# Performance work log

Measured on AMD Instinct MI355X. Metric: run time of the kernel, lower is better.

## Reference

```python
import jax, jax.numpy as jnp
import numpy as np

T, D_IN, H, KV, HD = 1024, 2048, 32, 8, 64
GROUP = H // KV  # 4
EPS = 1e-6


def _rmsnorm(x, w):
    inv_rms = jax.lax.rsqrt(jnp.mean(x * x, axis=-1, keepdims=True) + EPS)
    return x * inv_rms * w


def _rope(x, cos, sin):
    # x: [heads, T, HD]; cos/sin: [T, HD]
    hd = x.shape[-1]
    x1, x2 = x[..., : hd // 2], x[..., hd // 2 :]
    rotated = jnp.concatenate([-x2, x1], axis=-1)
    return x * cos[None, :, :] + rotated * sin[None, :, :]


def setup_inputs() -> dict:
    key = jax.random.key(0)
    ks = jax.random.split(key, 6)
    x = jax.random.normal(ks[0], (T, D_IN), dtype=jnp.float32)
    # RoPE tables (cos/sin over [T, HD])
    inv_freq = 1.0 / (10000.0 ** (np.arange(0, HD, 2, dtype=np.float64) / HD))
    ang = np.arange(T, dtype=np.float64)[:, None] * inv_freq[None, :]
    emb = np.concatenate([ang, ang], axis=-1)
    cos = jnp.asarray(np.cos(emb), dtype=jnp.float32)
    sin = jnp.asarray(np.sin(emb), dtype=jnp.float32)
    # causal mask: True above diagonal -> masked to -inf
    mask = jnp.triu(jnp.ones((T, T), dtype=jnp.bool_), k=1)
    # kaiming_normal fan_in (relu): std = sqrt(2/fan_in)
    Wq = jax.random.normal(ks[1], (H * HD, D_IN), jnp.float32) * (2.0 / D_IN) ** 0.5
    Wk = jax.random.normal(ks[2], (KV * HD, D_IN), jnp.float32) * (2.0 / D_IN) ** 0.5
    Wv = jax.random.normal(ks[3], (KV * HD, D_IN), jnp.float32) * (2.0 / D_IN) ** 0.5
    Wo = jax.random.normal(ks[4], (D_IN, H * HD), jnp.float32) * (2.0 / (H * HD)) ** 0.5
    q_norm_w = jnp.ones((HD,), jnp.float32)
    k_norm_w = jnp.ones((HD,), jnp.float32)
    one = jnp.ones((1,), jnp.float32)
    return {
        "x": x, "scale_x": one, "mask": mask,
        "cos": cos, "scale_cos": one, "sin": sin, "scale_sin": one,
        "Wq": Wq, "Wk": Wk, "Wv": Wv, "Wo": Wo,
        "q_norm_w": q_norm_w, "k_norm_w": k_norm_w,
    }


def reference(x, scale_x, mask, cos, scale_cos, sin, scale_sin,
              Wq, Wk, Wv, Wo, q_norm_w, k_norm_w):
    num_tokens = x.shape[0]
    # QKV projections
    q = (x @ Wq.T).reshape(num_tokens, H, HD).transpose(1, 0, 2)   # [H, T, HD]
    k = (x @ Wk.T).reshape(num_tokens, KV, HD).transpose(1, 0, 2)  # [KV, T, HD]
    v = (x @ Wv.T).reshape(num_tokens, KV, HD).transpose(1, 0, 2)  # [KV, T, HD]
    # qk_norm
    q = _rmsnorm(q, q_norm_w)
    k = _rmsnorm(k, k_norm_w)
    # RoPE
    q = _rope(q, cos, sin)
    k = _rope(k, cos, sin)
    # expand KV groups to all heads (repeat_interleave along head axis)
    k = jnp.repeat(k, GROUP, axis=0)  # [H, T, HD]
    v = jnp.repeat(v, GROUP, axis=0)  # [H, T, HD]
    # attention scores
    qk = jnp.einsum("htd,hsd->hts", q, k) / (HD ** 0.5)
    qk = jnp.where(mask[None, :, :], -jnp.inf, qk)
    attn = jax.nn.softmax(qk, axis=-1)
    out = jnp.einsum("hts,hsd->htd", attn, v)          # [H, T, HD]
    out = out.transpose(1, 0, 2).reshape(num_tokens, H * HD)
    return out @ Wo.T  # [T, D_IN]
```

## Files before the change

### kernel.cpp

```cpp
#include <hip/hip_runtime.h>

typedef __bf16 bf16x8 __attribute__((ext_vector_type(8)));
typedef float f32x4 __attribute__((ext_vector_type(4)));

#define T_TOK 1024
#define DIN   2048
#define NH    32
#define NKV   8
#define HD    64

__device__ __forceinline__ unsigned short f2bf(float f) {
  unsigned int u = __float_as_uint(f);
  unsigned int r = (u + 0x7fffu + ((u >> 16) & 1u)) >> 16;
  return (unsigned short)r;
}

__device__ __forceinline__ void glds16(const void* g, void* lds) {
  __builtin_amdgcn_global_load_lds(
      (const __attribute__((address_space(1))) void*)g,
      (__attribute__((address_space(3))) void*)lds, 16, 0, 0);
}

__global__ __launch_bounds__(256) void k_cvt_all(
    const float* __restrict__ x,  const float* __restrict__ wq,
    const float* __restrict__ wk, const float* __restrict__ wv,
    const float* __restrict__ wo, unsigned short* __restrict__ xb,
    unsigned short* __restrict__ wqkv, unsigned short* __restrict__ wob) {
  const long NX = 1l << 21, NWQ = 1l << 22, NWK = 1l << 20, NWV = 1l << 20;
  long i4 = ((long)blockIdx.x * blockDim.x + threadIdx.x) * 4;
  const float* src;
  unsigned short* dst;
  long off;
  if (i4 < NX)                       { src = x;  dst = xb;   off = i4; }
  else if (i4 < NX + NWQ)            { src = wq; dst = wqkv; off = i4 - NX; }
  else if (i4 < NX + NWQ + NWK)      { src = wk; dst = wqkv + NWQ; off = i4 - NX - NWQ; }
  else if (i4 < NX + NWQ + NWK + NWV){ src = wv; dst = wqkv + NWQ + NWK; off = i4 - NX - NWQ - NWK; }
  else                               { src = wo; dst = wob;  off = i4 - NX - NWQ - NWK - NWV; }
  float4 v = *reinterpret_cast<const float4*>(src + off);
  ushort4 o;
  o.x = f2bf(v.x); o.y = f2bf(v.y); o.z = f2bf(v.z); o.w = f2bf(v.w);
  *reinterpret_cast<ushort4*>(dst + off) = o;
}

template<int BM, int BN>
__global__ __launch_bounds__(256) void k_gemm2(
    const unsigned short* __restrict__ A, const unsigned short* __restrict__ B,
    float* __restrict__ C, int N, int K) {
  constexpr int NI = BM / 32;
  constexpr int NJ = BN / 32;
  __shared__ unsigned short As[2][BM * 64];
  __shared__ unsigned short Bs[2][BN * 64];
  const int lane = threadIdx.x & 63;
  const int wave = threadIdx.x >> 6;
  const int wm = wave >> 1, wn = wave & 1;
  const int lr = lane & 15, lk = lane >> 4;
  const int brow = blockIdx.y * BM;
  const int bcol = blockIdx.x * BN;

  const int srow = lane >> 3;
  const int scol = ((lane & 7) ^ srow) * 8;
  const unsigned short* Ag = A + (long)(brow + srow) * K + scol;
  const unsigned short* Bg = B + (long)(bcol + srow) * K + scol;

  f32x4 acc[NI][NJ];
#pragma unroll
  for (int i = 0; i < NI; i++)
#pragma unroll
    for (int j = 0; j < NJ; j++) acc[i][j] = (f32x4){0.f, 0.f, 0.f, 0.f};

  const int swz = (lr & 7) << 4;
  const int nt = K / 64;
  int cur = 0;

#pragma unroll
  for (int i = 0; i < NI; i++) {
    int strip = i * 4 + wave;
    glds16(Ag + (long)strip * 8 * K, (char*)As[0] + strip * 1024);
  }
#pragma unroll
  for (int i = 0; i < NJ; i++) {
    int strip = i * 4 + wave;
    glds16(Bg + (long)strip * 8 * K, (char*)Bs[0] + strip * 1024);
  }
  __syncthreads();

  for (int t = 0; t < nt; t++) {
    if (t + 1 < nt) {
      const int kk = (t + 1) * 64;
#pragma unroll
      for (int i = 0; i < NI; i++) {
        int strip = i * 4 + wave;
        glds16(Ag + (long)strip * 8 * K + kk, (char*)As[cur ^ 1] + strip * 1024);
      }
#pragma unroll
      for (int i = 0; i < NJ; i++) {
        int strip = i * 4 + wave;
        glds16(Bg + (long)strip * 8 * K + kk, (char*)Bs[cur ^ 1] + strip * 1024);
      }
    }
#pragma unroll
    for (int s = 0; s < 2; s++) {
      bf16x8 a[NI], b[NJ];
#pragma unroll
      for (int i = 0; i < NI; i++) {
        int row = wm * (BM / 2) + i * 16 + lr;
        a[i] = *reinterpret_cast<const bf16x8*>(
            (const char*)As[cur] + row * 128 + ((s * 64 + lk * 16) ^ swz));
      }
#pragma unroll
      for (int j = 0; j < NJ; j++) {
        int row = wn * (BN / 2) + j * 16 + lr;
        b[j] = *reinterpret_cast<const bf16x8*>(
            (const char*)Bs[cur] + row * 128 + ((s * 64 + lk * 16) ^ swz));
      }
#pragma unroll
      for (int i = 0; i < NI; i++)
#pragma unroll
        for (int j = 0; j < NJ; j++)
          acc[i][j] = __builtin_amdgcn_mfma_f32_16x16x32_bf16(a[i], b[j], acc[i][j], 0, 0, 0);
    }
    __syncthreads();
    cur ^= 1;
  }

#pragma unroll
  for (int i = 0; i < NI; i++)
#pragma unroll
    for (int j = 0; j < NJ; j++)
#pragma unroll
      for (int p = 0; p < 4; p++)
        C[(long)(brow + wm * (BM / 2) + i * 16 + lk * 4 + p) * N +
          (bcol + wn * (BN / 2) + j * 16 + lr)] = acc[i][j][p];
}

__global__ void k_norm_rope(const float* __restrict__ qkv_lin,
                            unsigned short* __restrict__ qb, unsigned short* __restrict__ kb,
                            const float* __restrict__ cosT, const float* __restrict__ sinT,
                            const float* __restrict__ qw, const float* __restrict__ kw) {
  int gw = (blockIdx.x * blockDim.x + threadIdx.x) >> 6;
  int lane = threadIdx.x & 63;
  int t = gw / (NH + NKV);
  int hh = gw % (NH + NKV);
  if (t >= T_TOK) return;
  const float* base;
  unsigned short* ob;
  const float* w;
  if (hh < NH) {
    base = qkv_lin + (long)t * 3072 + hh * HD;
    ob   = qb + (long)t * (NH * HD) + hh * HD;
    w = qw;
  } else {
    int kh = hh - NH;
    base = qkv_lin + (long)t * 3072 + 2048 + kh * HD;
    ob   = kb + (long)t * (NKV * HD) + kh * HD;
    w = kw;
  }
  float v = base[lane];
  float ss = v * v;
#pragma unroll
  for (int off = 1; off < 64; off <<= 1) ss += __shfl_xor(ss, off);
  float xn = v * rsqrtf(ss * (1.0f / HD) + 1e-6f) * w[lane];
  float other = __shfl_xor(xn, 32);
  float c = cosT[t * HD + lane], s = sinT[t * HD + lane];
  ob[lane] = f2bf(xn * c + (lane < 32 ? -other : other) * s);
}

__global__ __launch_bounds__(256) void k_vt(const float* __restrict__ qkv_lin,
                                            unsigned short* __restrict__ out) {
  __shared__ float t[32][33];
  int tx = threadIdx.x & 31, ty = threadIdx.x >> 5;
  int r0 = blockIdx.y * 32;
  int c0 = blockIdx.x * 32;
#pragma unroll
  for (int r = 0; r < 4; r++)
    t[ty + r * 8][tx] = qkv_lin[(long)(r0 + ty + r * 8) * 3072 + 2560 + c0 + tx];
  __syncthreads();
#pragma unroll
  for (int r = 0; r < 4; r++)
    out[(long)(c0 + ty + r * 8) * 1024 + r0 + tx] = f2bf(t[tx][ty + r * 8]);
}

__global__ __launch_bounds__(256) void k_flash(
    const unsigned short* __restrict__ qb, const unsigned short* __restrict__ kb,
    const unsigned short* __restrict__ vtb, unsigned short* __restrict__ ao) {
  __shared__ unsigned short Ks[2][64 * 64];
  __shared__ unsigned short Vs[2][64 * 64];
  __shared__ unsigned short plds[4][16 * 64];
  const int rb = 63 - blockIdx.x;
  const int kvh = blockIdx.y;
  const int lane = threadIdx.x & 63;
  const int wave = threadIdx.x >> 6;
  const int h = kvh * 4 + wave;
  const int lr = lane & 15, lk = lane >> 4;
  const int qrow = rb * 16;
  const int qt = rb >> 2;
  const int qrel = (rb & 3) * 16 + lr;
  const int pswz = (lr & 7) << 4;
  char* pbase = (char*)plds[wave];
  const float SC = 0.125f * 1.44269504f;
  const f32x4 z4 = {0.f, 0.f, 0.f, 0.f};

  const int srow = lane >> 3;
  const int scol = ((lane & 7) ^ srow) * 8;

#define STAGE(buf, tt) do {                                                    \
    _Pragma("unroll") for (int s_ = 0; s_ < 2; s_++) {                         \
      int strip = s_ * 4 + wave;                                               \
      glds16(kb + (long)((tt) * 64 + strip * 8 + srow) * 512 + kvh * 64 + scol,\
             (char*)Ks[buf] + strip * 1024);                                   \
      glds16(vtb + (long)(kvh * 64 + strip * 8 + srow) * 1024 + (tt) * 64 + scol,\
             (char*)Vs[buf] + strip * 1024);                                   \
    }                                                                          \
  } while (0)

  const unsigned short* qp = qb + (long)(qrow + lr) * (NH * HD) + h * HD + lk * 8;
  bf16x8 qa0 = *reinterpret_cast<const bf16x8*>(qp);
  bf16x8 qa1 = *reinterpret_cast<const bf16x8*>(qp + 32);

  f32x4 o[4];
#pragma unroll
  for (int f = 0; f < 4; f++) o[f] = z4;
  float m2 = -3.0e38f;
  float lp = 0.f;

  const int ntiles = qt + 1;
  int cur = 0;
  STAGE(0, 0);
  __syncthreads();

  for (int t = 0; t < ntiles; t++) {
    if (t + 1 < ntiles) STAGE(cur ^ 1, t + 1);
    bf16x8 kf0[4], kf1[4];
#pragma unroll
    for (int f = 0; f < 4; f++) {
      const char* kbase = (const char*)Ks[cur] + (f * 16 + lr) * 128;
      kf0[f] = *reinterpret_cast<const bf16x8*>(kbase + ((lk * 16) ^ pswz));
      kf1[f] = *reinterpret_cast<const bf16x8*>(kbase + ((64 + lk * 16) ^ pswz));
    }
    f32x4 sacc[4];
    __builtin_amdgcn_s_setprio(1);
#pragma unroll
    for (int f = 0; f < 4; f++) {
      sacc[f] = __builtin_amdgcn_mfma_f32_16x16x32_bf16(kf0[f], qa0, z4, 0, 0, 0);
      sacc[f] = __builtin_amdgcn_mfma_f32_16x16x32_bf16(kf1[f], qa1, sacc[f], 0, 0, 0);
    }
    __builtin_amdgcn_s_setprio(0);
    const bool diag = (t == qt);
    float tmax = -3.0e38f;
#pragma unroll
    for (int f = 0; f < 4; f++)
#pragma unroll
      for (int p = 0; p < 4; p++) {
        float s_ = sacc[f][p] * SC;
        if (diag && (f * 16 + lk * 4 + p) > qrel) s_ = -3.0e38f;
        sacc[f][p] = s_;
        tmax = fmaxf(tmax, s_);
      }
    tmax = fmaxf(tmax, __shfl_xor(tmax, 16));
    tmax = fmaxf(tmax, __shfl_xor(tmax, 32));
    float mn = fmaxf(m2, tmax);
    float r = exp2f(m2 - mn);
    m2 = mn;
    float rp[4];
#pragma unroll
    for (int p = 0; p < 4; p++)
      rp[p] = __shfl(r, (lane & 48) | (lk * 4 + p));
    float ps = 0.f;
#pragma unroll
    for (int f = 0; f < 4; f++) {
      float e0 = exp2f(sacc[f][0] - mn), e1 = exp2f(sacc[f][1] - mn);
      float e2 = exp2f(sacc[f][2] - mn), e3 = exp2f(sacc[f][3] - mn);
      ps += (e0 + e1) + (e2 + e3);
      uint2 pk;
      pk.x = (unsigned)f2bf(e0) | ((unsigned)f2bf(e1) << 16);
      pk.y = (unsigned)f2bf(e2) | ((unsigned)f2bf(e3) << 16);
      *reinterpret_cast<uint2*>(pbase + lr * 128 + ((f * 32 + lk * 8) ^ pswz)) = pk;
    }
    lp = lp * r + ps;
#pragma unroll
    for (int fd = 0; fd < 4; fd++)
#pragma unroll
      for (int p = 0; p < 4; p++) o[fd][p] *= rp[p];
    bf16x8 vfr[8];
#pragma unroll
    for (int fd = 0; fd < 4; fd++) {
      const char* vbase = (const char*)Vs[cur] + (fd * 16 + lr) * 128;
      vfr[fd]     = *reinterpret_cast<const bf16x8*>(vbase + ((lk * 16) ^ pswz));
      vfr[4 + fd] = *reinterpret_cast<const bf16x8*>(vbase + ((64 + lk * 16) ^ pswz));
    }
    __builtin_amdgcn_s_setprio(1);
#pragma unroll
    for (int ks = 0; ks < 2; ks++) {
      bf16x8 pa = *reinterpret_cast<const bf16x8*>(
          pbase + lr * 128 + ((ks * 64 + lk * 16) ^ pswz));
#pragma unroll
      for (int fd = 0; fd < 4; fd++)
        o[fd] = __builtin_amdgcn_mfma_f32_16x16x32_bf16(pa, vfr[ks * 4 + fd], o[fd], 0, 0, 0);
    }
    __builtin_amdgcn_s_setprio(0);
    __syncthreads();
    cur ^= 1;
  }

  lp += __shfl_xor(lp, 16);
  lp += __shfl_xor(lp, 32);
  float lo[4];
#pragma unroll
  for (int p = 0; p < 4; p++) lo[p] = __shfl(lp, (lane & 48) | (lk * 4 + p));
#pragma unroll
  for (int fd = 0; fd < 4; fd++)
#pragma unroll
    for (int p = 0; p < 4; p++) {
      int qg = qrow + lk * 4 + p;
      int d = fd * 16 + lr;
      ao[(long)qg * (NH * HD) + h * HD + d] = f2bf(o[fd][p] / lo[p]);
    }
#undef STAGE
}

extern "C" void kernel_launch(void* const* d_in, const int* in_sizes, int n_in,
                              void* d_out, int out_size, void* d_ws, size_t ws_size,
                              hipStream_t stream) {
  const float* x    = (const float*)d_in[0];
  const float* cosT = (const float*)d_in[3];
  const float* sinT = (const float*)d_in[5];
  const float* Wq   = (const float*)d_in[7];
  const float* Wk   = (const float*)d_in[8];
  const float* Wv   = (const float*)d_in[9];
  const float* Wo   = (const float*)d_in[10];
  const float* qw   = (const float*)d_in[11];
  const float* kw   = (const float*)d_in[12];
  float* out = (float*)d_out;

  char* ws = (char*)d_ws;
  unsigned short* xb    = (unsigned short*)(ws);
  unsigned short* Wqkv  = (unsigned short*)(ws + (4u << 20));
  unsigned short* Wob   = (unsigned short*)(ws + (16u << 20));
  float* qkv_lin = (float*)(ws + (24u << 20));
  unsigned short* qbb = (unsigned short*)(ws + (36u << 20));
  unsigned short* kbb = (unsigned short*)(ws + (40u << 20));
  unsigned short* vtb = (unsigned short*)(ws + (41u << 20));
  unsigned short* ao  = (unsigned short*)(ws + (42u << 20));

  k_cvt_all<<<12288, 256, 0, stream>>>(x, Wq, Wk, Wv, Wo, xb, Wqkv, Wob);

  k_gemm2<128, 128><<<dim3(24, 8), 256, 0, stream>>>(xb, Wqkv, qkv_lin, 3072, 2048);

  k_norm_rope<<<(T_TOK * (NH + NKV) * 64) / 256, 256, 0, stream>>>(
      qkv_lin, qbb, kbb, cosT, sinT, qw, kw);

  k_vt<<<dim3(16, 32), 256, 0, stream>>>(qkv_lin, vtb);

  k_flash<<<dim3(64, 8), 256, 0, stream>>>(qbb, kbb, vtb, ao);

  k_gemm2<128, 128><<<dim3(16, 8), 256, 0, stream>>>(ao, Wob, out, 2048, 2048);
}
```

Before: 220.7 us.

## Deepen GEMM and flash-attention LDS pipelines to four buffers with explicit vmcnt waits

Both the bf16 GEMM and the flash-attention kernel move from double-buffered to 4-slot LDS ring buffers with three tiles prefetched ahead. The per-iteration __syncthreads is replaced by explicit s_waitcnt vmcnt counts plus a single s_barrier, so later async loads can stay in flight while the current tile is computed. MFMA sections get raised wave priority. This hides more global-load latency at the cost of doubled LDS usage, and it relies on the hand-set vmcnt values matching the exact number of issued loads.

```diff
diff --git a/kernel.cpp b/kernel.cpp
--- a/kernel.cpp
+++ b/kernel.cpp
@@ -43,13 +43,13 @@
 }
 
 template<int BM, int BN>
-__global__ __launch_bounds__(256) void k_gemm2(
+__global__ __launch_bounds__(256) void k_gemm3(
     const unsigned short* __restrict__ A, const unsigned short* __restrict__ B,
     float* __restrict__ C, int N, int K) {
   constexpr int NI = BM / 32;
   constexpr int NJ = BN / 32;
-  __shared__ unsigned short As[2][BM * 64];
-  __shared__ unsigned short Bs[2][BN * 64];
+  __shared__ unsigned short As[4][BM * 64];
+  __shared__ unsigned short Bs[4][BN * 64];
   const int lane = threadIdx.x & 63;
   const int wave = threadIdx.x >> 6;
   const int wm = wave >> 1, wn = wave & 1;
@@ -70,34 +70,31 @@
 
   const int swz = (lr & 7) << 4;
   const int nt = K / 64;
-  int cur = 0;
-
-#pragma unroll
-  for (int i = 0; i < NI; i++) {
-    int strip = i * 4 + wave;
-    glds16(Ag + (long)strip * 8 * K, (char*)As[0] + strip * 1024);
-  }
-#pragma unroll
-  for (int i = 0; i < NJ; i++) {
-    int strip = i * 4 + wave;
-    glds16(Bg + (long)strip * 8 * K, (char*)Bs[0] + strip * 1024);
-  }
-  __syncthreads();
+
+#define GSTAGE(buf, tt) do {                                                   \
+    const int kk_ = (tt) * 64;                                                 \
+    _Pragma("unroll") for (int i_ = 0; i_ < NI; i_++) {                        \
+      int strip = i_ * 4 + wave;                                               \
+      glds16(Ag + (long)strip * 8 * K + kk_, (char*)As[buf] + strip * 1024);   \
+    }                                                                          \
+    _Pragma("unroll") for (int i_ = 0; i_ < NJ; i_++) {                        \
+      int strip = i_ * 4 + wave;                                               \
+      glds16(Bg + (long)strip * 8 * K + kk_, (char*)Bs[buf] + strip * 1024);   \
+    }                                                                          \
+  } while (0)
+
+  GSTAGE(0, 0);
+  GSTAGE(1, 1);
+  GSTAGE(2, 2);
 
   for (int t = 0; t < nt; t++) {
-    if (t + 1 < nt) {
-      const int kk = (t + 1) * 64;
-#pragma unroll
-      for (int i = 0; i < NI; i++) {
-        int strip = i * 4 + wave;
-        glds16(Ag + (long)strip * 8 * K + kk, (char*)As[cur ^ 1] + strip * 1024);
-      }
-#pragma unroll
-      for (int i = 0; i < NJ; i++) {
-        int strip = i * 4 + wave;
-        glds16(Bg + (long)strip * 8 * K + kk, (char*)Bs[cur ^ 1] + strip * 1024);
-      }
-    }
+    if (t + 2 < nt)      { asm volatile("s_waitcnt vmcnt(16)" ::: "memory"); }
+    else if (t + 1 < nt) { asm volatile("s_waitcnt vmcnt(8)"  ::: "memory"); }
+    else                 { asm volatile("s_waitcnt vmcnt(0)"  ::: "memory"); }
+    __builtin_amdgcn_sched_barrier(0);
+    __builtin_amdgcn_s_barrier();
+    if (t + 3 < nt) GSTAGE((t + 3) & 3, t + 3);
+    const int cur = t & 3;
 #pragma unroll
     for (int s = 0; s < 2; s++) {
       bf16x8 a[NI], b[NJ];
@@ -113,15 +110,16 @@
         b[j] = *reinterpret_cast<const bf16x8*>(
             (const char*)Bs[cur] + row * 128 + ((s * 64 + lk * 16) ^ swz));
       }
+      __builtin_amdgcn_s_setprio(1);
 #pragma unroll
       for (int i = 0; i < NI; i++)
 #pragma unroll
         for (int j = 0; j < NJ; j++)
           acc[i][j] = __builtin_amdgcn_mfma_f32_16x16x32_bf16(a[i], b[j], acc[i][j], 0, 0, 0);
-    }
-    __syncthreads();
-    cur ^= 1;
+      __builtin_amdgcn_s_setprio(0);
+    }
   }
+#undef GSTAGE
 
 #pragma unroll
   for (int i = 0; i < NI; i++)
@@ -183,8 +181,8 @@
 __global__ __launch_bounds__(256) void k_flash(
     const unsigned short* __restrict__ qb, const unsigned short* __restrict__ kb,
     const unsigned short* __restrict__ vtb, unsigned short* __restrict__ ao) {
-  __shared__ unsigned short Ks[2][64 * 64];
-  __shared__ unsigned short Vs[2][64 * 64];
+  __shared__ unsigned short Ks[4][64 * 64];
+  __shared__ unsigned short Vs[4][64 * 64];
   __shared__ unsigned short plds[4][16 * 64];
   const int rb = 63 - blockIdx.x;
   const int kvh = blockIdx.y;
@@ -224,12 +222,18 @@
   float lp = 0.f;
 
   const int ntiles = qt + 1;
-  int cur = 0;
   STAGE(0, 0);
-  __syncthreads();
+  if (ntiles > 1) STAGE(1, 1);
+  if (ntiles > 2) STAGE(2, 2);
 
   for (int t = 0; t < ntiles; t++) {
-    if (t + 1 < ntiles) STAGE(cur ^ 1, t + 1);
+    if (t + 2 < ntiles)      { asm volatile("s_waitcnt vmcnt(8)" ::: "memory"); }
+    else if (t + 1 < ntiles) { asm volatile("s_waitcnt vmcnt(4)" ::: "memory"); }
+    else                     { asm volatile("s_waitcnt vmcnt(0)" ::: "memory"); }
+    __builtin_amdgcn_sched_barrier(0);
+    __builtin_amdgcn_s_barrier();
+    if (t + 3 < ntiles) STAGE((t + 3) & 3, t + 3);
+    const int cur = t & 3;
     bf16x8 kf0[4], kf1[4];
 #pragma unroll
     for (int f = 0; f < 4; f++) {
@@ -298,9 +302,8 @@
         o[fd] = __builtin_amdgcn_mfma_f32_16x16x32_bf16(pa, vfr[ks * 4 + fd], o[fd], 0, 0, 0);
     }
     __builtin_amdgcn_s_setprio(0);
-    __syncthreads();
-    cur ^= 1;
   }
+#undef STAGE
 
   lp += __shfl_xor(lp, 16);
   lp += __shfl_xor(lp, 32);
@@ -315,7 +318,6 @@
       int d = fd * 16 + lr;
       ao[(long)qg * (NH * HD) + h * HD + d] = f2bf(o[fd][p] / lo[p]);
     }
-#undef STAGE
 }
 
 extern "C" void kernel_launch(void* const* d_in, const int* in_sizes, int n_in,
@@ -344,7 +346,7 @@
 
   k_cvt_all<<<12288, 256, 0, stream>>>(x, Wq, Wk, Wv, Wo, xb, Wqkv, Wob);
 
-  k_gemm2<128, 128><<<dim3(24, 8), 256, 0, stream>>>(xb, Wqkv, qkv_lin, 3072, 2048);
+  k_gemm3<128, 128><<<dim3(24, 8), 256, 0, stream>>>(xb, Wqkv, qkv_lin, 3072, 2048);
 
   k_norm_rope<<<(T_TOK * (NH + NKV) * 64) / 256, 256, 0, stream>>>(
       qkv_lin, qbb, kbb, cosT, sinT, qw, kw);
@@ -353,5 +355,5 @@
 
   k_flash<<<dim3(64, 8), 256, 0, stream>>>(qbb, kbb, vtb, ao);
 
-  k_gemm2<128, 128><<<dim3(16, 8), 256, 0, stream>>>(ao, Wob, out, 2048, 2048);
-}
+  k_gemm3<128, 128><<<dim3(16, 8), 256, 0, stream>>>(ao, Wob, out, 2048, 2048);
+}
```

New measurement: 218.9 us. About the same (-0.8%).
